# Performance work log

Measured on AMD Instinct MI355X. Metric: run time of the kernel, lower is better.

Reference implementation:

```python
import jax, jax.numpy as jnp
import numpy as np
from jax import lax

V, E, H = 10000, 512, 512
B, L, T = 128, 8, 48


def setup_inputs() -> dict:
    key = jax.random.key(0)
    ks = jax.random.split(key, 12)
    s = lambda k, shape: jax.random.normal(k, shape, jnp.float32) * 0.05
    kw_lens = jnp.sort(jax.random.randint(ks[2], (B,), 1, L + 1))[::-1]  # descending, as pack_padded requires
    return {
        "kws": jax.random.randint(ks[0], (B, L), 0, V),
        "poem": jax.random.randint(ks[1], (B, T), 0, V),
        "kw_lens": kw_lens,
        "embedding": s(ks[3], (V, E)),
        "enc_Wih": s(ks[4], (4 * H, E)), "enc_Whh": s(ks[5], (4 * H, H)), "enc_b": s(ks[6], (4 * H,)),
        "dec_Wih": s(ks[7], (4 * H, E)), "dec_Whh": s(ks[8], (4 * H, H)), "dec_b": s(ks[9], (4 * H,)),
        "out_W": s(ks[10], (V, 2 * H)), "out_b": s(ks[11], (V,)),
    }


def _lstm_step(h, c, x, Wih, Whh, b):
    # PyTorch gate order: i, f, g, o
    gates = x @ Wih.T + h @ Whh.T + b  # [B, 4H]
    i, f, g, o = jnp.split(gates, 4, axis=-1)
    c = jax.nn.sigmoid(f) * c + jax.nn.sigmoid(i) * jnp.tanh(g)
    h = jax.nn.sigmoid(o) * jnp.tanh(c)
    return h, c


def reference(kws, poem, kw_lens, embedding, enc_Wih, enc_Whh, enc_b,
              dec_Wih, dec_Whh, dec_b, out_W, out_b):
    bs = kws.shape[0]
    mask = jnp.arange(L)[None, :] < kw_lens[:, None]  # sequence_mask, [B, L]

    # ---- encoder LSTM over keywords (dropout inactive at eval) ----
    kws_emb = embedding[kws]  # [B, L, E]

    def enc_scan(carry, x):
        h, c = carry
        h, c = _lstm_step(h, c, x, enc_Wih, enc_Whh, enc_b)
        return (h, c), (h, c)

    z = jnp.zeros((bs, H), embedding.dtype)
    _, (hs, cs) = lax.scan(enc_scan, (z, z), kws_emb.transpose(1, 0, 2))  # [L, B, H]
    kws_rep = hs.transpose(1, 0, 2) * mask[..., None]  # pad_packed zeros past length
    # pack semantics: final hidden is the state at the last valid timestep
    bidx = jnp.arange(bs)
    h0 = hs[kw_lens - 1, bidx]
    c0 = cs[kw_lens - 1, bidx]

    # ---- greedy per-timestep decode with dot-product attention ----
    neg = jnp.asarray(-1e9, embedding.dtype)

    def dec_scan(carry, tok):
        h, c = carry
        x = embedding[tok]  # [B, E]
        h, c = _lstm_step(h, c, x, dec_Wih, dec_Whh, dec_b)
        scores = jnp.einsum('bh,blh->bl', h, kws_rep)
        attn = jax.nn.softmax(jnp.where(mask, scores, neg), axis=-1)
        ctx = jnp.einsum('bl,blh->bh', attn, kws_rep)
        logits = jnp.concatenate([h, ctx], axis=-1) @ out_W.T + out_b  # [B, V]
        return (h, c), logits

    _, preds = lax.scan(dec_scan, (h0, c0), poem.T)  # [T, B, V]
    return preds.transpose(1, 0, 2)  # [B, T, V]
```

## Files before the change

kernel.cpp:

```cpp
#include <hip/hip_runtime.h>
#include <hip/hip_bf16.h>

typedef __bf16 bf16;
typedef __attribute__((ext_vector_type(8))) __bf16 bf16x8;
typedef __attribute__((ext_vector_type(4))) __bf16 bf16x4;
typedef __attribute__((ext_vector_type(4))) float f32x4;

#define B_ 128
#define L_ 8
#define T_ 48
#define V_ 10000
#define NBLK_REC 32

__device__ __forceinline__ float sigf(float x) { return 1.f / (1.f + expf(-x)); }

__device__ __forceinline__ void gl_lds16(const bf16* g, bf16* l) {
  __builtin_amdgcn_global_load_lds(
      (const __attribute__((address_space(1))) unsigned int*)g,
      (__attribute__((address_space(3))) unsigned int*)l, 16, 0, 0);
}

__device__ __forceinline__ unsigned aload32(const void* p) {
  return __hip_atomic_load((unsigned*)p, __ATOMIC_RELAXED, __HIP_MEMORY_SCOPE_AGENT);
}
__device__ __forceinline__ void astore64(void* p, unsigned long long v) {
  __hip_atomic_store((unsigned long long*)p, v, __ATOMIC_RELAXED, __HIP_MEMORY_SCOPE_AGENT);
}
__device__ __forceinline__ float bflo(unsigned u) { return __uint_as_float(u << 16); }
__device__ __forceinline__ float bfhi(unsigned u) { return __uint_as_float(u & 0xffff0000u); }
__device__ __forceinline__ unsigned packbf(float lo, float hi) {
  bf16 a = (bf16)lo, b = (bf16)hi;
  unsigned short ua = __builtin_bit_cast(unsigned short, a);
  unsigned short ub = __builtin_bit_cast(unsigned short, b);
  return (unsigned)ua | ((unsigned)ub << 16);
}

__device__ __forceinline__ void signal(unsigned* flg, int blk, unsigned step) {
  asm volatile("s_waitcnt vmcnt(0)" ::: "memory");
  __syncthreads();
  if (threadIdx.x == 0)
    __hip_atomic_store(flg + blk * 32, step, __ATOMIC_RELAXED, __HIP_MEMORY_SCOPE_AGENT);
}
__device__ __forceinline__ void waitstep(const unsigned* flg, unsigned step) {
  if (threadIdx.x < 64) {
    int lane = threadIdx.x;
    for (;;) {
      unsigned v = (lane < NBLK_REC) ? aload32(flg + lane * 32) : step;
      if (__all((int)(v >= step))) break;
      __builtin_amdgcn_s_sleep(1);
    }
  }
  __syncthreads();
}

__global__ void prep_kernel(
    const int* __restrict__ kws, const int* __restrict__ poem,
    const float* __restrict__ emb,
    const float* __restrict__ eWih, const float* __restrict__ eWhh,
    const float* __restrict__ dWih, const float* __restrict__ dWhh,
    const float* __restrict__ outW,
    bf16* __restrict__ WihE, bf16* __restrict__ WhhE,
    bf16* __restrict__ WihD, bf16* __restrict__ WhhD,
    bf16* __restrict__ outWb,
    bf16* __restrict__ Xenc, bf16* __restrict__ Xdec,
    unsigned* __restrict__ flg)
{
  if (blockIdx.x == 0)
    for (int i = threadIdx.x; i < 1024; i += blockDim.x) flg[i] = 0u;
  const long SW = 1048576;
  const long SOWP = 10354688;
  const long SXE = 524288;
  const long SXD = 3145728;
  const long total = 4 * SW + SOWP + SXE + SXD;
  for (long i = blockIdx.x * (long)blockDim.x + threadIdx.x; i < total;
       i += (long)gridDim.x * blockDim.x) {
    long j = i;
    if (j < SW) { WihE[j] = (bf16)eWih[j]; continue; } j -= SW;
    if (j < SW) { WhhE[j] = (bf16)eWhh[j]; continue; } j -= SW;
    if (j < SW) { WihD[j] = (bf16)dWih[j]; continue; } j -= SW;
    if (j < SW) { WhhD[j] = (bf16)dWhh[j]; continue; } j -= SW;
    if (j < SOWP) {
      long r = j >> 10;
      outWb[j] = (r < 10000) ? (bf16)outW[j] : (bf16)0.f;
      continue;
    } j -= SOWP;
    if (j < SXE) {
      int e = (int)(j & 511); int b = (int)((j >> 9) & 127); int l = (int)(j >> 16);
      int tok = kws[b * L_ + l];
      Xenc[j] = (bf16)emb[(long)tok * 512 + e];
      continue;
    } j -= SXE;
    {
      int e = (int)(j & 511); int b = (int)((j >> 9) & 127); int t = (int)(j >> 16);
      int tok = poem[b * T_ + t];
      Xdec[j] = (bf16)emb[(long)tok * 512 + e];
    }
  }
}

template<int MODE>
__global__ __launch_bounds__(256) void gemm2_kernel(
    const bf16* __restrict__ A, const bf16* __restrict__ Bm,
    const float* __restrict__ bias, void* __restrict__ outp,
    int M, int N, int K, int MT)
{
  __shared__ bf16 As[128 * 32];
  __shared__ bf16 Bs[128 * 32];
  const int tid = threadIdx.x, lane = tid & 63, wid = tid >> 6;
  const int nwg = gridDim.x;
  int bid = blockIdx.x;
  int tm, tn;
  if (MODE == 2) {
    int xcd = bid & 7, idx = bid >> 3;
    tm = xcd * 6 + idx % 6;
    tn = idx / 6;
  } else {
    int swz = ((nwg & 7) == 0) ? ((bid & 7) * (nwg >> 3) + (bid >> 3)) : bid;
    tm = swz % MT; tn = swz / MT;
  }
  const int m0 = tm * 128, n0 = tn * 128;
  const int wm = (wid >> 1) * 64, wn = (wid & 1) * 64;
  const int fr = lane & 15, ku = lane >> 4;

  f32x4 acc[4][4];
  #pragma unroll
  for (int mi = 0; mi < 4; ++mi)
    #pragma unroll
    for (int ni = 0; ni < 4; ++ni) {
      acc[mi][ni][0] = 0.f; acc[mi][ni][1] = 0.f;
      acc[mi][ni][2] = 0.f; acc[mi][ni][3] = 0.f;
    }

  for (int kt = 0; kt < K; kt += 32) {
    #pragma unroll
    for (int j = 0; j < 2; ++j) {
      int i0 = j * 256 + wid * 64;
      int i = i0 + lane;
      int r = i >> 2, ub = i & 3;
      gl_lds16(A + (size_t)(m0 + r) * K + kt + ub * 8, As + (size_t)i0 * 8);
      gl_lds16(Bm + (size_t)(n0 + r) * K + kt + ub * 8, Bs + (size_t)i0 * 8);
    }
    __syncthreads();
    bf16x8 af[4], bfr[4];
    #pragma unroll
    for (int mi = 0; mi < 4; ++mi)
      af[mi] = *(const bf16x8*)(As + (size_t)(wm + mi * 16 + fr) * 32 + ku * 8);
    #pragma unroll
    for (int ni = 0; ni < 4; ++ni)
      bfr[ni] = *(const bf16x8*)(Bs + (size_t)(wn + ni * 16 + fr) * 32 + ku * 8);
    #pragma unroll
    for (int mi = 0; mi < 4; ++mi)
      #pragma unroll
      for (int ni = 0; ni < 4; ++ni)
        acc[mi][ni] = __builtin_amdgcn_mfma_f32_16x16x32_bf16(af[mi], bfr[ni], acc[mi][ni], 0, 0, 0);
    __syncthreads();
  }

  const int fq = (lane >> 4) * 4;
  #pragma unroll
  for (int mi = 0; mi < 4; ++mi) {
    #pragma unroll
    for (int ni = 0; ni < 4; ++ni) {
      #pragma unroll
      for (int j = 0; j < 4; ++j) {
        int r = m0 + wm + mi * 16 + fq + j;
        int cix = n0 + wn + ni * 16 + fr;
        if (cix < N) {
          float v = acc[mi][ni][j] + bias[cix];
          if (MODE == 2) {
            int b = r & 127, t = r >> 7;
            ((float*)outp)[(size_t)b * (T_ * V_) + (size_t)t * V_ + cix] = v;
          } else {
            ((bf16*)outp)[((size_t)(r >> 7) * 2048 + cix) * 128 + (r & 127)] = (bf16)v;
          }
        }
      }
    }
  }
}

__global__ __launch_bounds__(256, 1) void recurrent_kernel(
    const bf16* __restrict__ preEncT, const bf16* __restrict__ preDecT,
    const bf16* __restrict__ WhhE, const bf16* __restrict__ WhhD,
    const int* __restrict__ kwl,
    bf16* __restrict__ hS,
    bf16* __restrict__ h0b,
    bf16* __restrict__ hsEnc,
    bf16* __restrict__ Hcat,
    unsigned* __restrict__ flg)
{
  __shared__ bf16 Bs[64 * 512];
  __shared__ bf16 As[128 * 256];
  const int tid = threadIdx.x, lane = tid & 63, wid = tid >> 6;
  const int blk = blockIdx.x, n0 = blk * 16;
  const int fr = lane & 15, fq = (lane >> 4) * 4, ku = lane >> 4;
  const int axor = fr & 7;
  const int arow0 = wid * 32 + fr, arow1 = wid * 32 + 16 + fr;
  const int row0 = wid * 32 + fq, row1 = wid * 32 + 16 + fq;
  const int brow = tid >> 1, bhalf = tid & 1;
  const int blen = kwl[brow];
  const int batt = blk * 4 + wid;
  const int lenb = kwl[batt];
  int lenr[2][4];
  #pragma unroll
  for (int j = 0; j < 4; ++j) { lenr[0][j] = kwl[row0 + j]; lenr[1][j] = kwl[row1 + j]; }

  auto loadB = [&](const bf16* W) {
    #pragma unroll
    for (int j = 0; j < 16; ++j) {
      int i = j * 256 + tid;
      int r = i >> 6, u = i & 63;
      int p = u ^ (r & 7);
      bf16x8 v = *(const bf16x8*)(W + (size_t)((r >> 4) * 512 + n0 + (r & 15)) * 512 + u * 8);
      *(bf16x8*)(Bs + (size_t)r * 512 + p * 8) = v;
    }
  };

  f32x4 acc[2][4];
  auto zacc = [&]() {
    #pragma unroll
    for (int mi = 0; mi < 2; ++mi)
      #pragma unroll
      for (int g = 0; g < 4; ++g) {
        acc[mi][g][0] = 0.f; acc[mi][g][1] = 0.f;
        acc[mi][g][2] = 0.f; acc[mi][g][3] = 0.f;
      }
  };

  auto gemm_full = [&](const bf16* h_in) {
    #pragma unroll
    for (int ch = 0; ch < 2; ++ch) {
      f32x4 tv[16];
      #pragma unroll
      for (int j = 0; j < 16; ++j) {
        int i = j * 256 + tid;
        int r = i >> 5, up = i & 31;
        const bf16* ga = h_in + (size_t)r * 512 + ch * 256 + up * 8;
        asm volatile("global_load_dwordx4 %0, %1, off sc0 sc1"
                     : "=v"(tv[j]) : "v"(ga) : "memory");
      }
      asm volatile("s_waitcnt vmcnt(0)" ::: "memory");
      __builtin_amdgcn_sched_barrier(0);
      #pragma unroll
      for (int j = 0; j < 16; ++j) {
        int i = j * 256 + tid;
        int r = i >> 5, up = i & 31;
        int s = up ^ (r & 7);
        *(f32x4*)(As + ((size_t)r * 32 + s) * 8) = tv[j];
      }
      __syncthreads();
      #pragma unroll
      for (int kt = 0; kt < 8; ++kt) {
        int cA = (kt * 4 + ku) ^ axor;
        int cB = ((ch * 8 + kt) * 4 + ku) ^ axor;
        bf16x8 af0 = *(const bf16x8*)(As + (size_t)arow0 * 256 + cA * 8);
        bf16x8 af1 = *(const bf16x8*)(As + (size_t)arow1 * 256 + cA * 8);
        #pragma unroll
        for (int g = 0; g < 4; ++g) {
          bf16x8 bv = *(const bf16x8*)(Bs + (size_t)(g * 16 + fr) * 512 + cB * 8);
          acc[0][g] = __builtin_amdgcn_mfma_f32_16x16x32_bf16(af0, bv, acc[0][g], 0, 0, 0);
          acc[1][g] = __builtin_amdgcn_mfma_f32_16x16x32_bf16(af1, bv, acc[1][g], 0, 0, 0);
        }
      }
      __syncthreads();
    }
  };

  float cr[2][4] = {{0.f,0.f,0.f,0.f},{0.f,0.f,0.f,0.f}};
  float c0r[2][4] = {{0.f,0.f,0.f,0.f},{0.f,0.f,0.f,0.f}};
  bf16 hout[2][4];

  bf16x4 gv[2][4];
  auto prefg = [&](const bf16* preT) {
    #pragma unroll
    for (int mi = 0; mi < 2; ++mi) {
      int rbase = mi ? row1 : row0;
      int hcol = n0 + fr;
      #pragma unroll
      for (int g = 0; g < 4; ++g)
        gv[mi][g] = *(const bf16x4*)(preT + ((size_t)(g * 512 + hcol)) * 128 + rbase);
    }
  };

  auto pointwise = [&]() {
    #pragma unroll
    for (int mi = 0; mi < 2; ++mi) {
      #pragma unroll
      for (int j = 0; j < 4; ++j) {
        float gi = acc[mi][0][j] + (float)gv[mi][0][j];
        float gf = acc[mi][1][j] + (float)gv[mi][1][j];
        float gg = acc[mi][2][j] + (float)gv[mi][2][j];
        float go = acc[mi][3][j] + (float)gv[mi][3][j];
        float cn = sigf(gf) * cr[mi][j] + sigf(gi) * tanhf(gg);
        float hn = sigf(go) * tanhf(cn);
        cr[mi][j] = cn;
        hout[mi][j] = (bf16)hn;
      }
    }
  };

  auto bounce_store = [&](bf16* hdst, bf16* hsdst, int t, int is_enc) {
    #pragma unroll
    for (int mi = 0; mi < 2; ++mi) {
      int rbase = mi ? row1 : row0;
      #pragma unroll
      for (int j = 0; j < 4; ++j)
        As[(size_t)(rbase + j) * 16 + fr] = hout[mi][j];
    }
    __syncthreads();
    unsigned long long v0 = *(unsigned long long*)(As + (size_t)brow * 16 + bhalf * 8);
    unsigned long long v1 = *(unsigned long long*)(As + (size_t)brow * 16 + bhalf * 8 + 4);
    size_t off = (size_t)brow * 512 + n0 + bhalf * 8;
    astore64(hdst + off, v0);
    astore64(hdst + off + 4, v1);
    if (is_enc) {
      unsigned long long m0 = (t < blen) ? v0 : 0ull;
      unsigned long long m1 = (t < blen) ? v1 : 0ull;
      astore64(hsdst + off, m0);
      astore64(hsdst + off + 4, m1);
      if (t == blen - 1) {
        astore64(h0b + off, v0);
        astore64(h0b + off + 4, v1);
      }
    }
  };

  unsigned hatt[4];
  auto load_hatt = [&](const bf16* h_in) {
    #pragma unroll
    for (int e = 0; e < 4; ++e)
      hatt[e] = aload32(h_in + (size_t)batt * 512 + lane * 2 + 128 * e);
  };

  unsigned hsr[8][4];

  auto attention = [&](int tprev) {
    float sc[8];
    #pragma unroll
    for (int l = 0; l < 8; ++l) {
      float p = 0.f;
      #pragma unroll
      for (int e = 0; e < 4; ++e)
        p += bflo(hatt[e]) * bflo(hsr[l][e]) + bfhi(hatt[e]) * bfhi(hsr[l][e]);
      #pragma unroll
      for (int off = 32; off; off >>= 1) p += __shfl_xor(p, off);
      sc[l] = p;
    }
    float m = -1e30f;
    #pragma unroll
    for (int l = 0; l < 8; ++l) m = fmaxf(m, (l < lenb) ? sc[l] : -1e30f);
    float wgt[8]; float den = 0.f;
    #pragma unroll
    for (int l = 0; l < 8; ++l) { wgt[l] = (l < lenb) ? expf(sc[l] - m) : 0.f; den += wgt[l]; }
    float inv = 1.f / den;
    bf16* dst = Hcat + ((size_t)tprev * 128 + batt) * 1024;
    #pragma unroll
    for (int e = 0; e < 4; ++e) {
      float clo = 0.f, chi = 0.f;
      #pragma unroll
      for (int l = 0; l < 8; ++l) {
        clo += wgt[l] * bflo(hsr[l][e]);
        chi += wgt[l] * bfhi(hsr[l][e]);
      }
      *(unsigned*)(dst + 512 + lane * 2 + 128 * e) = packbf(clo * inv, chi * inv);
      *(unsigned*)(dst + lane * 2 + 128 * e) = hatt[e];
    }
  };

  loadB(WhhE);
  __syncthreads();
  for (int t = 0; t < 8; ++t) {
    prefg(preEncT + (size_t)t * 262144);
    zacc();
    if (t > 0) {
      waitstep(flg, (unsigned)t);
      gemm_full(hS + (size_t)(t - 1) * 65536);
    }
    pointwise();
    #pragma unroll
    for (int mi = 0; mi < 2; ++mi)
      #pragma unroll
      for (int j = 0; j < 4; ++j)
        if (t == lenr[mi][j] - 1) c0r[mi][j] = cr[mi][j];
    bounce_store(hS + (size_t)t * 65536, hsEnc + (size_t)t * 65536, t, 1);
    signal(flg, blk, (unsigned)(t + 1));
  }

  __syncthreads();
  loadB(WhhD);
  __syncthreads();
  waitstep(flg, 8u);
  #pragma unroll
  for (int l = 0; l < 8; ++l)
    #pragma unroll
    for (int e = 0; e < 4; ++e)
      hsr[l][e] = aload32(hsEnc + ((size_t)l * 128 + batt) * 512 + lane * 2 + 128 * e);
  #pragma unroll
  for (int mi = 0; mi < 2; ++mi)
    #pragma unroll
    for (int j = 0; j < 4; ++j) cr[mi][j] = c0r[mi][j];

  for (int t = 0; t < 48; ++t) {
    prefg(preDecT + (size_t)t * 262144);
    zacc();
    const bf16* hin = (t == 0) ? (const bf16*)h0b : (const bf16*)(hS + (size_t)(8 + t - 1) * 65536);
    waitstep(flg, (unsigned)(8 + t));
    gemm_full(hin);
    pointwise();
    bounce_store(hS + (size_t)(8 + t) * 65536, nullptr, t, 0);
    signal(flg, blk, (unsigned)(9 + t));
    if (t >= 1) {
      load_hatt(hin);
      attention(t - 1);
    }
  }
  waitstep(flg, 56u);
  load_hatt(hS + (size_t)55 * 65536);
  attention(47);
}

extern "C" void kernel_launch(void* const* d_in, const int* in_sizes, int n_in,
                              void* d_out, int out_size, void* d_ws, size_t ws_size,
                              hipStream_t stream)
{
  const int* kws  = (const int*)d_in[0];
  const int* poem = (const int*)d_in[1];
  const int* kwl  = (const int*)d_in[2];
  const float* emb  = (const float*)d_in[3];
  const float* eWih = (const float*)d_in[4];
  const float* eWhh = (const float*)d_in[5];
  const float* eb   = (const float*)d_in[6];
  const float* dWih = (const float*)d_in[7];
  const float* dWhh = (const float*)d_in[8];
  const float* db   = (const float*)d_in[9];
  const float* outW = (const float*)d_in[10];
  const float* outb = (const float*)d_in[11];
  float* out = (float*)d_out;

  char* base = (char*)d_ws;
  size_t o = 0;
  auto take = [&](size_t bytes) -> char* {
    char* r = base + o;
    o += (bytes + 255) & ~(size_t)255;
    return r;
  };
  bf16* WihE  = (bf16*)take(2048 * 512 * 2);
  bf16* WhhE  = (bf16*)take(2048 * 512 * 2);
  bf16* WihD  = (bf16*)take(2048 * 512 * 2);
  bf16* WhhD  = (bf16*)take(2048 * 512 * 2);
  bf16* outWb = (bf16*)take((size_t)10112 * 1024 * 2);
  bf16* Xenc  = (bf16*)take(1024 * 512 * 2);
  bf16* Xdec  = (bf16*)take((size_t)6144 * 512 * 2);
  bf16* preEncT = (bf16*)take((size_t)8 * 2048 * 128 * 2);
  bf16* preDecT = (bf16*)take((size_t)48 * 2048 * 128 * 2);
  bf16* Hcat   = (bf16*)take((size_t)6144 * 1024 * 2);
  bf16* hS     = (bf16*)take((size_t)56 * 65536 * 2);
  bf16* hsEnc  = (bf16*)take((size_t)8 * 128 * 512 * 2);
  bf16* h0b    = (bf16*)take(128 * 512 * 2);
  unsigned* flg = (unsigned*)take(4096);

  prep_kernel<<<4096, 256, 0, stream>>>(kws, poem, emb, eWih, eWhh, dWih, dWhh, outW,
                                        WihE, WhhE, WihD, WhhD, outWb, Xenc, Xdec, flg);

  gemm2_kernel<3><<<128, 256, 0, stream>>>(Xenc, WihE, eb, preEncT, 1024, 2048, 512, 8);
  gemm2_kernel<3><<<768, 256, 0, stream>>>(Xdec, WihD, db, preDecT, 6144, 2048, 512, 48);

  recurrent_kernel<<<NBLK_REC, 256, 0, stream>>>(preEncT, preDecT, WhhE, WhhD, kwl,
                                                 hS, h0b, hsEnc, Hcat, flg);

  gemm2_kernel<2><<<3792, 256, 0, stream>>>(Hcat, outWb, outb, out, 6144, 10000, 1024, 48);
}
```

Measured before the change: 788.1 us.

## Fuse decoder input GEMM and output projection into persistent recurrent kernel

Merges the decoder input-projection GEMM and the vocabulary output GEMM into the recurrent kernel. The kernel launches 240 blocks: 32 run the LSTM recurrence and 208 worker blocks first compute preDecT and then stream the output-logit tiles per timestep as soon as that step's Hcat rows are flagged complete. The goal is to overlap the large output GEMM and the decoder pre-GEMM with the latency-bound serial recurrence, and to remove kernel launch gaps. In exchange it relies on all 240 blocks being co-resident for the spin-wait flags, and the worker GEMM loses the XCD-aware tile swizzle and uses a simpler unpipelined load path.

```diff
diff --git a/kernel.cpp b/kernel.cpp
--- a/kernel.cpp
+++ b/kernel.cpp
@@ -11,6 +11,8 @@
 #define T_ 48
 #define V_ 10000
 #define NBLK_REC 32
+#define NBLK_TOT 240
+#define NW (NBLK_TOT - NBLK_REC)
 
 __device__ __forceinline__ float sigf(float x) { return 1.f / (1.f + expf(-x)); }
 
@@ -33,24 +35,6 @@
   unsigned short ua = __builtin_bit_cast(unsigned short, a);
   unsigned short ub = __builtin_bit_cast(unsigned short, b);
   return (unsigned)ua | ((unsigned)ub << 16);
-}
-
-__device__ __forceinline__ void signal(unsigned* flg, int blk, unsigned step) {
-  asm volatile("s_waitcnt vmcnt(0)" ::: "memory");
-  __syncthreads();
-  if (threadIdx.x == 0)
-    __hip_atomic_store(flg + blk * 32, step, __ATOMIC_RELAXED, __HIP_MEMORY_SCOPE_AGENT);
-}
-__device__ __forceinline__ void waitstep(const unsigned* flg, unsigned step) {
-  if (threadIdx.x < 64) {
-    int lane = threadIdx.x;
-    for (;;) {
-      unsigned v = (lane < NBLK_REC) ? aload32(flg + lane * 32) : step;
-      if (__all((int)(v >= step))) break;
-      __builtin_amdgcn_s_sleep(1);
-    }
-  }
-  __syncthreads();
 }
 
 __global__ void prep_kernel(
@@ -63,10 +47,10 @@
     bf16* __restrict__ WihD, bf16* __restrict__ WhhD,
     bf16* __restrict__ outWb,
     bf16* __restrict__ Xenc, bf16* __restrict__ Xdec,
-    unsigned* __restrict__ flg)
+    unsigned* __restrict__ ctl)
 {
   if (blockIdx.x == 0)
-    for (int i = threadIdx.x; i < 1024; i += blockDim.x) flg[i] = 0u;
+    for (int i = threadIdx.x; i < 8192; i += blockDim.x) ctl[i] = 0u;
   const long SW = 1048576;
   const long SOWP = 10354688;
   const long SXE = 524288;
@@ -98,10 +82,9 @@
   }
 }
 
-template<int MODE>
-__global__ __launch_bounds__(256) void gemm2_kernel(
+__global__ __launch_bounds__(256) void gemm_pre_kernel(
     const bf16* __restrict__ A, const bf16* __restrict__ Bm,
-    const float* __restrict__ bias, void* __restrict__ outp,
+    const float* __restrict__ bias, bf16* __restrict__ outp,
     int M, int N, int K, int MT)
 {
   __shared__ bf16 As[128 * 32];
@@ -109,15 +92,8 @@
   const int tid = threadIdx.x, lane = tid & 63, wid = tid >> 6;
   const int nwg = gridDim.x;
   int bid = blockIdx.x;
-  int tm, tn;
-  if (MODE == 2) {
-    int xcd = bid & 7, idx = bid >> 3;
-    tm = xcd * 6 + idx % 6;
-    tn = idx / 6;
-  } else {
-    int swz = ((nwg & 7) == 0) ? ((bid & 7) * (nwg >> 3) + (bid >> 3)) : bid;
-    tm = swz % MT; tn = swz / MT;
-  }
+  int swz = ((nwg & 7) == 0) ? ((bid & 7) * (nwg >> 3) + (bid >> 3)) : bid;
+  const int tm = swz % MT, tn = swz / MT;
   const int m0 = tm * 128, n0 = tn * 128;
   const int wm = (wid >> 1) * 64, wn = (wid & 1) * 64;
   const int fr = lane & 15, ku = lane >> 4;
@@ -165,258 +141,454 @@
       for (int j = 0; j < 4; ++j) {
         int r = m0 + wm + mi * 16 + fq + j;
         int cix = n0 + wn + ni * 16 + fr;
-        if (cix < N) {
-          float v = acc[mi][ni][j] + bias[cix];
-          if (MODE == 2) {
-            int b = r & 127, t = r >> 7;
-            ((float*)outp)[(size_t)b * (T_ * V_) + (size_t)t * V_ + cix] = v;
-          } else {
-            ((bf16*)outp)[((size_t)(r >> 7) * 2048 + cix) * 128 + (r & 127)] = (bf16)v;
-          }
-        }
+        outp[((size_t)(r >> 7) * 2048 + cix) * 128 + (r & 127)] = (bf16)(acc[mi][ni][j] + bias[cix]);
       }
     }
   }
 }
 
-__global__ __launch_bounds__(256, 1) void recurrent_kernel(
-    const bf16* __restrict__ preEncT, const bf16* __restrict__ preDecT,
+__global__ __launch_bounds__(256, 1) void fused_kernel(
+    const bf16* __restrict__ preEncT, bf16* __restrict__ preDecT,
     const bf16* __restrict__ WhhE, const bf16* __restrict__ WhhD,
     const int* __restrict__ kwl,
-    bf16* __restrict__ hS,
-    bf16* __restrict__ h0b,
-    bf16* __restrict__ hsEnc,
-    bf16* __restrict__ Hcat,
-    unsigned* __restrict__ flg)
+    bf16* __restrict__ hS, bf16* __restrict__ h0b,
+    bf16* __restrict__ hsEnc, bf16* __restrict__ Hcat,
+    const bf16* __restrict__ Xdec, const bf16* __restrict__ WihD,
+    const float* __restrict__ db, const bf16* __restrict__ outWb,
+    const float* __restrict__ outb, float* __restrict__ out,
+    unsigned* __restrict__ ctl)
 {
-  __shared__ bf16 Bs[64 * 512];
-  __shared__ bf16 As[128 * 256];
+  __shared__ __align__(16) char pool[131072];
   const int tid = threadIdx.x, lane = tid & 63, wid = tid >> 6;
-  const int blk = blockIdx.x, n0 = blk * 16;
-  const int fr = lane & 15, fq = (lane >> 4) * 4, ku = lane >> 4;
-  const int axor = fr & 7;
-  const int arow0 = wid * 32 + fr, arow1 = wid * 32 + 16 + fr;
-  const int row0 = wid * 32 + fq, row1 = wid * 32 + 16 + fq;
-  const int brow = tid >> 1, bhalf = tid & 1;
-  const int blen = kwl[brow];
-  const int batt = blk * 4 + wid;
-  const int lenb = kwl[batt];
-  int lenr[2][4];
-  #pragma unroll
-  for (int j = 0; j < 4; ++j) { lenr[0][j] = kwl[row0 + j]; lenr[1][j] = kwl[row1 + j]; }
-
-  auto loadB = [&](const bf16* W) {
-    #pragma unroll
-    for (int j = 0; j < 16; ++j) {
-      int i = j * 256 + tid;
-      int r = i >> 6, u = i & 63;
-      int p = u ^ (r & 7);
-      bf16x8 v = *(const bf16x8*)(W + (size_t)((r >> 4) * 512 + n0 + (r & 15)) * 512 + u * 8);
-      *(bf16x8*)(Bs + (size_t)r * 512 + p * 8) = v;
-    }
-  };
-
-  f32x4 acc[2][4];
-  auto zacc = [&]() {
-    #pragma unroll
-    for (int mi = 0; mi < 2; ++mi)
-      #pragma unroll
-      for (int g = 0; g < 4; ++g) {
-        acc[mi][g][0] = 0.f; acc[mi][g][1] = 0.f;
-        acc[mi][g][2] = 0.f; acc[mi][g][3] = 0.f;
-      }
-  };
-
-  auto gemm_full = [&](const bf16* h_in) {
-    #pragma unroll
-    for (int ch = 0; ch < 2; ++ch) {
-      f32x4 tv[16];
+
+  if (blockIdx.x < NBLK_REC) {
+    bf16* Bs = (bf16*)pool;
+    bf16* As = (bf16*)(pool + 65536);
+    unsigned* flg = ctl;
+    const int blk = blockIdx.x, n0 = blk * 16;
+    const int fr = lane & 15, fq = (lane >> 4) * 4, ku = lane >> 4;
+    const int axor = fr & 7;
+    const int arow0 = wid * 32 + fr, arow1 = wid * 32 + 16 + fr;
+    const int row0 = wid * 32 + fq, row1 = wid * 32 + 16 + fq;
+    const int brow = tid >> 1, bhalf = tid & 1;
+    const int blen = kwl[brow];
+    const int batt = blk * 4 + wid;
+    const int lenb = kwl[batt];
+    int lenr[2][4];
+    #pragma unroll
+    for (int j = 0; j < 4; ++j) { lenr[0][j] = kwl[row0 + j]; lenr[1][j] = kwl[row1 + j]; }
+
+    auto signal = [&](unsigned step) {
+      asm volatile("s_waitcnt vmcnt(0)" ::: "memory");
+      __syncthreads();
+      if (tid == 0)
+        __hip_atomic_store(flg + blk * 32, step, __ATOMIC_RELAXED, __HIP_MEMORY_SCOPE_AGENT);
+    };
+    auto waitstep = [&](unsigned step) {
+      if (tid < 64) {
+        int l = tid;
+        for (;;) {
+          unsigned v = (l < NBLK_REC) ? aload32(flg + l * 32) : step;
+          if (__all((int)(v >= step))) break;
+          __builtin_amdgcn_s_sleep(1);
+        }
+      }
+      __syncthreads();
+    };
+
+    auto loadB = [&](const bf16* W) {
       #pragma unroll
       for (int j = 0; j < 16; ++j) {
         int i = j * 256 + tid;
-        int r = i >> 5, up = i & 31;
-        const bf16* ga = h_in + (size_t)r * 512 + ch * 256 + up * 8;
-        asm volatile("global_load_dwordx4 %0, %1, off sc0 sc1"
-                     : "=v"(tv[j]) : "v"(ga) : "memory");
-      }
+        int r = i >> 6, u = i & 63;
+        int p = u ^ (r & 7);
+        bf16x8 v = *(const bf16x8*)(W + (size_t)((r >> 4) * 512 + n0 + (r & 15)) * 512 + u * 8);
+        *(bf16x8*)(Bs + (size_t)r * 512 + p * 8) = v;
+      }
+    };
+
+    f32x4 acc[2][4];
+    auto zacc = [&]() {
+      #pragma unroll
+      for (int mi = 0; mi < 2; ++mi)
+        #pragma unroll
+        for (int g = 0; g < 4; ++g) {
+          acc[mi][g][0] = 0.f; acc[mi][g][1] = 0.f;
+          acc[mi][g][2] = 0.f; acc[mi][g][3] = 0.f;
+        }
+    };
+
+    auto gemm_full = [&](const bf16* h_in) {
+      #pragma unroll
+      for (int ch = 0; ch < 2; ++ch) {
+        f32x4 tv[16];
+        #pragma unroll
+        for (int j = 0; j < 16; ++j) {
+          int i = j * 256 + tid;
+          int r = i >> 5, up = i & 31;
+          const bf16* ga = h_in + (size_t)r * 512 + ch * 256 + up * 8;
+          asm volatile("global_load_dwordx4 %0, %1, off sc0 sc1"
+                       : "=v"(tv[j]) : "v"(ga) : "memory");
+        }
+        asm volatile("s_waitcnt vmcnt(0)" ::: "memory");
+        __builtin_amdgcn_sched_barrier(0);
+        #pragma unroll
+        for (int j = 0; j < 16; ++j) {
+          int i = j * 256 + tid;
+          int r = i >> 5, up = i & 31;
+          int s = up ^ (r & 7);
+          *(f32x4*)(As + ((size_t)r * 32 + s) * 8) = tv[j];
+        }
+        __syncthreads();
+        #pragma unroll
+        for (int kt = 0; kt < 8; ++kt) {
+          int cA = (kt * 4 + ku) ^ axor;
+          int cB = ((ch * 8 + kt) * 4 + ku) ^ axor;
+          bf16x8 af0 = *(const bf16x8*)(As + (size_t)arow0 * 256 + cA * 8);
+          bf16x8 af1 = *(const bf16x8*)(As + (size_t)arow1 * 256 + cA * 8);
+          #pragma unroll
+          for (int g = 0; g < 4; ++g) {
+            bf16x8 bv = *(const bf16x8*)(Bs + (size_t)(g * 16 + fr) * 512 + cB * 8);
+            acc[0][g] = __builtin_amdgcn_mfma_f32_16x16x32_bf16(af0, bv, acc[0][g], 0, 0, 0);
+            acc[1][g] = __builtin_amdgcn_mfma_f32_16x16x32_bf16(af1, bv, acc[1][g], 0, 0, 0);
+          }
+        }
+        __syncthreads();
+      }
+    };
+
+    float cr[2][4] = {{0.f,0.f,0.f,0.f},{0.f,0.f,0.f,0.f}};
+    float c0r[2][4] = {{0.f,0.f,0.f,0.f},{0.f,0.f,0.f,0.f}};
+    bf16 hout[2][4];
+    bf16x4 gv[2][4];
+
+    auto prefg = [&](const bf16* preT) {
+      #pragma unroll
+      for (int mi = 0; mi < 2; ++mi) {
+        int rbase = mi ? row1 : row0;
+        int hcol = n0 + fr;
+        #pragma unroll
+        for (int g = 0; g < 4; ++g)
+          gv[mi][g] = *(const bf16x4*)(preT + ((size_t)(g * 512 + hcol)) * 128 + rbase);
+      }
+    };
+    auto prefg_c = [&](const bf16* preT) {
+      #pragma unroll
+      for (int mi = 0; mi < 2; ++mi) {
+        int rbase = mi ? row1 : row0;
+        int hcol = n0 + fr;
+        #pragma unroll
+        for (int g = 0; g < 4; ++g) {
+          const bf16* p = preT + ((size_t)(g * 512 + hcol)) * 128 + rbase;
+          unsigned long long u;
+          asm volatile("global_load_dwordx2 %0, %1, off sc0 sc1" : "=v"(u) : "v"(p) : "memory");
+          gv[mi][g] = __builtin_bit_cast(bf16x4, u);
+        }
+      }
+    };
+
+    auto pointwise = [&]() {
+      #pragma unroll
+      for (int mi = 0; mi < 2; ++mi) {
+        #pragma unroll
+        for (int j = 0; j < 4; ++j) {
+          float gi = acc[mi][0][j] + (float)gv[mi][0][j];
+          float gf = acc[mi][1][j] + (float)gv[mi][1][j];
+          float gg = acc[mi][2][j] + (float)gv[mi][2][j];
+          float go = acc[mi][3][j] + (float)gv[mi][3][j];
+          float cn = sigf(gf) * cr[mi][j] + sigf(gi) * tanhf(gg);
+          float hn = sigf(go) * tanhf(cn);
+          cr[mi][j] = cn;
+          hout[mi][j] = (bf16)hn;
+        }
+      }
+    };
+
+    auto bounce_store = [&](bf16* hdst, bf16* hsdst, int t, int is_enc) {
+      #pragma unroll
+      for (int mi = 0; mi < 2; ++mi) {
+        int rbase = mi ? row1 : row0;
+        #pragma unroll
+        for (int j = 0; j < 4; ++j)
+          As[(size_t)(rbase + j) * 16 + fr] = hout[mi][j];
+      }
+      __syncthreads();
+      unsigned long long v0 = *(unsigned long long*)(As + (size_t)brow * 16 + bhalf * 8);
+      unsigned long long v1 = *(unsigned long long*)(As + (size_t)brow * 16 + bhalf * 8 + 4);
+      size_t off = (size_t)brow * 512 + n0 + bhalf * 8;
+      astore64(hdst + off, v0);
+      astore64(hdst + off + 4, v1);
+      if (is_enc) {
+        unsigned long long m0 = (t < blen) ? v0 : 0ull;
+        unsigned long long m1 = (t < blen) ? v1 : 0ull;
+        astore64(hsdst + off, m0);
+        astore64(hsdst + off + 4, m1);
+        if (t == blen - 1) {
+          astore64(h0b + off, v0);
+          astore64(h0b + off + 4, v1);
+        }
+      }
+    };
+
+    unsigned hatt[4];
+    auto load_hatt = [&](const bf16* h_in) {
+      #pragma unroll
+      for (int e = 0; e < 4; ++e) {
+        const bf16* p = h_in + (size_t)batt * 512 + lane * 2 + 128 * e;
+        asm volatile("global_load_dword %0, %1, off sc0 sc1" : "=v"(hatt[e]) : "v"(p) : "memory");
+      }
+    };
+
+    unsigned hsr[8][4];
+
+    auto attention = [&](int tprev) {
       asm volatile("s_waitcnt vmcnt(0)" ::: "memory");
       __builtin_amdgcn_sched_barrier(0);
-      #pragma unroll
-      for (int j = 0; j < 16; ++j) {
-        int i = j * 256 + tid;
-        int r = i >> 5, up = i & 31;
-        int s = up ^ (r & 7);
-        *(f32x4*)(As + ((size_t)r * 32 + s) * 8) = tv[j];
-      }
-      __syncthreads();
-      #pragma unroll
-      for (int kt = 0; kt < 8; ++kt) {
-        int cA = (kt * 4 + ku) ^ axor;
-        int cB = ((ch * 8 + kt) * 4 + ku) ^ axor;
-        bf16x8 af0 = *(const bf16x8*)(As + (size_t)arow0 * 256 + cA * 8);
-        bf16x8 af1 = *(const bf16x8*)(As + (size_t)arow1 * 256 + cA * 8);
-        #pragma unroll
-        for (int g = 0; g < 4; ++g) {
-          bf16x8 bv = *(const bf16x8*)(Bs + (size_t)(g * 16 + fr) * 512 + cB * 8);
-          acc[0][g] = __builtin_amdgcn_mfma_f32_16x16x32_bf16(af0, bv, acc[0][g], 0, 0, 0);
-          acc[1][g] = __builtin_amdgcn_mfma_f32_16x16x32_bf16(af1, bv, acc[1][g], 0, 0, 0);
-        }
-      }
-      __syncthreads();
-    }
-  };
-
-  float cr[2][4] = {{0.f,0.f,0.f,0.f},{0.f,0.f,0.f,0.f}};
-  float c0r[2][4] = {{0.f,0.f,0.f,0.f},{0.f,0.f,0.f,0.f}};
-  bf16 hout[2][4];
-
-  bf16x4 gv[2][4];
-  auto prefg = [&](const bf16* preT) {
-    #pragma unroll
-    for (int mi = 0; mi < 2; ++mi) {
-      int rbase = mi ? row1 : row0;
-      int hcol = n0 + fr;
-      #pragma unroll
-      for (int g = 0; g < 4; ++g)
-        gv[mi][g] = *(const bf16x4*)(preT + ((size_t)(g * 512 + hcol)) * 128 + rbase);
-    }
-  };
-
-  auto pointwise = [&]() {
-    #pragma unroll
-    for (int mi = 0; mi < 2; ++mi) {
-      #pragma unroll
-      for (int j = 0; j < 4; ++j) {
-        float gi = acc[mi][0][j] + (float)gv[mi][0][j];
-        float gf = acc[mi][1][j] + (float)gv[mi][1][j];
-        float gg = acc[mi][2][j] + (float)gv[mi][2][j];
-        float go = acc[mi][3][j] + (float)gv[mi][3][j];
-        float cn = sigf(gf) * cr[mi][j] + sigf(gi) * tanhf(gg);
-        float hn = sigf(go) * tanhf(cn);
-        cr[mi][j] = cn;
-        hout[mi][j] = (bf16)hn;
-      }
-    }
-  };
-
-  auto bounce_store = [&](bf16* hdst, bf16* hsdst, int t, int is_enc) {
-    #pragma unroll
-    for (int mi = 0; mi < 2; ++mi) {
-      int rbase = mi ? row1 : row0;
-      #pragma unroll
-      for (int j = 0; j < 4; ++j)
-        As[(size_t)(rbase + j) * 16 + fr] = hout[mi][j];
-    }
+      float sc[8];
+      #pragma unroll
+      for (int l = 0; l < 8; ++l) {
+        float p = 0.f;
+        #pragma unroll
+        for (int e = 0; e < 4; ++e)
+          p += bflo(hatt[e]) * bflo(hsr[l][e]) + bfhi(hatt[e]) * bfhi(hsr[l][e]);
+        #pragma unroll
+        for (int off = 32; off; off >>= 1) p += __shfl_xor(p, off);
+        sc[l] = p;
+      }
+      float m = -1e30f;
+      #pragma unroll
+      for (int l = 0; l < 8; ++l) m = fmaxf(m, (l < lenb) ? sc[l] : -1e30f);
+      float wgt[8]; float den = 0.f;
+      #pragma unroll
+      for (int l = 0; l < 8; ++l) { wgt[l] = (l < lenb) ? expf(sc[l] - m) : 0.f; den += wgt[l]; }
+      float inv = 1.f / den;
+      bf16* dst = Hcat + ((size_t)tprev * 128 + batt) * 1024;
+      #pragma unroll
+      for (int e = 0; e < 4; ++e) {
+        float clo = 0.f, chi = 0.f;
+        #pragma unroll
+        for (int l = 0; l < 8; ++l) {
+          clo += wgt[l] * bflo(hsr[l][e]);
+          chi += wgt[l] * bfhi(hsr[l][e]);
+        }
+        unsigned cw = packbf(clo * inv, chi * inv);
+        unsigned* d1 = (unsigned*)(dst + 512 + lane * 2 + 128 * e);
+        unsigned* d0 = (unsigned*)(dst + lane * 2 + 128 * e);
+        asm volatile("global_store_dword %0, %1, off sc0 sc1" :: "v"(d1), "v"(cw) : "memory");
+        asm volatile("global_store_dword %0, %1, off sc0 sc1" :: "v"(d0), "v"(hatt[e]) : "memory");
+      }
+    };
+
+    auto hcat_done = [&](int t) {
+      asm volatile("s_waitcnt vmcnt(0)" ::: "memory");
+      __syncthreads();
+      if (tid == 0)
+        __hip_atomic_fetch_add(ctl + 1056 + t * 32, 1u, __ATOMIC_RELAXED, __HIP_MEMORY_SCOPE_AGENT);
+    };
+
+    loadB(WhhE);
     __syncthreads();
-    unsigned long long v0 = *(unsigned long long*)(As + (size_t)brow * 16 + bhalf * 8);
-    unsigned long long v1 = *(unsigned long long*)(As + (size_t)brow * 16 + bhalf * 8 + 4);
-    size_t off = (size_t)brow * 512 + n0 + bhalf * 8;
-    astore64(hdst + off, v0);
-    astore64(hdst + off + 4, v1);
-    if (is_enc) {
-      unsigned long long m0 = (t < blen) ? v0 : 0ull;
-      unsigned long long m1 = (t < blen) ? v1 : 0ull;
-      astore64(hsdst + off, m0);
-      astore64(hsdst + off + 4, m1);
-      if (t == blen - 1) {
-        astore64(h0b + off, v0);
-        astore64(h0b + off + 4, v1);
-      }
-    }
-  };
-
-  unsigned hatt[4];
-  auto load_hatt = [&](const bf16* h_in) {
-    #pragma unroll
-    for (int e = 0; e < 4; ++e)
-      hatt[e] = aload32(h_in + (size_t)batt * 512 + lane * 2 + 128 * e);
-  };
-
-  unsigned hsr[8][4];
-
-  auto attention = [&](int tprev) {
-    float sc[8];
-    #pragma unroll
-    for (int l = 0; l < 8; ++l) {
-      float p = 0.f;
+    for (int t = 0; t < 8; ++t) {
+      prefg(preEncT + (size_t)t * 262144);
+      zacc();
+      if (t > 0) {
+        waitstep((unsigned)t);
+        gemm_full(hS + (size_t)(t - 1) * 65536);
+      }
+      pointwise();
+      #pragma unroll
+      for (int mi = 0; mi < 2; ++mi)
+        #pragma unroll
+        for (int j = 0; j < 4; ++j)
+          if (t == lenr[mi][j] - 1) c0r[mi][j] = cr[mi][j];
+      bounce_store(hS + (size_t)t * 65536, hsEnc + (size_t)t * 65536, t, 1);
+      signal((unsigned)(t + 1));
+    }
+
+    __syncthreads();
+    loadB(WhhD);
+    __syncthreads();
+    waitstep(8u);
+    #pragma unroll
+    for (int l = 0; l < 8; ++l)
       #pragma unroll
       for (int e = 0; e < 4; ++e)
-        p += bflo(hatt[e]) * bflo(hsr[l][e]) + bfhi(hatt[e]) * bfhi(hsr[l][e]);
-      #pragma unroll
-      for (int off = 32; off; off >>= 1) p += __shfl_xor(p, off);
-      sc[l] = p;
-    }
-    float m = -1e30f;
-    #pragma unroll
-    for (int l = 0; l < 8; ++l) m = fmaxf(m, (l < lenb) ? sc[l] : -1e30f);
-    float wgt[8]; float den = 0.f;
-    #pragma unroll
-    for (int l = 0; l < 8; ++l) { wgt[l] = (l < lenb) ? expf(sc[l] - m) : 0.f; den += wgt[l]; }
-    float inv = 1.f / den;
-    bf16* dst = Hcat + ((size_t)tprev * 128 + batt) * 1024;
-    #pragma unroll
-    for (int e = 0; e < 4; ++e) {
-      float clo = 0.f, chi = 0.f;
-      #pragma unroll
-      for (int l = 0; l < 8; ++l) {
-        clo += wgt[l] * bflo(hsr[l][e]);
-        chi += wgt[l] * bfhi(hsr[l][e]);
-      }
-      *(unsigned*)(dst + 512 + lane * 2 + 128 * e) = packbf(clo * inv, chi * inv);
-      *(unsigned*)(dst + lane * 2 + 128 * e) = hatt[e];
-    }
-  };
-
-  loadB(WhhE);
-  __syncthreads();
-  for (int t = 0; t < 8; ++t) {
-    prefg(preEncT + (size_t)t * 262144);
-    zacc();
-    if (t > 0) {
-      waitstep(flg, (unsigned)t);
-      gemm_full(hS + (size_t)(t - 1) * 65536);
-    }
-    pointwise();
+        hsr[l][e] = aload32(hsEnc + ((size_t)l * 128 + batt) * 512 + lane * 2 + 128 * e);
     #pragma unroll
     for (int mi = 0; mi < 2; ++mi)
       #pragma unroll
-      for (int j = 0; j < 4; ++j)
-        if (t == lenr[mi][j] - 1) c0r[mi][j] = cr[mi][j];
-    bounce_store(hS + (size_t)t * 65536, hsEnc + (size_t)t * 65536, t, 1);
-    signal(flg, blk, (unsigned)(t + 1));
+      for (int j = 0; j < 4; ++j) cr[mi][j] = c0r[mi][j];
+    if (tid == 0) {
+      unsigned v; int it = 0;
+      do {
+        asm volatile("global_load_dword %0, %1, off sc0 sc1\ns_waitcnt vmcnt(0)"
+                     : "=v"(v) : "v"(ctl + 1024) : "memory");
+        if (v >= 768u) break;
+        __builtin_amdgcn_s_sleep(4);
+      } while (++it < (1 << 20));
+    }
+    __syncthreads();
+
+    for (int t = 0; t < 48; ++t) {
+      prefg_c(preDecT + (size_t)t * 262144);
+      zacc();
+      const bf16* hin = (t == 0) ? (const bf16*)h0b
+                                 : (const bf16*)(hS + (size_t)(8 + t - 1) * 65536);
+      waitstep((unsigned)(8 + t));
+      gemm_full(hin);
+      pointwise();
+      bounce_store(hS + (size_t)(8 + t) * 65536, nullptr, t, 0);
+      signal((unsigned)(9 + t));
+      if (t >= 1) {
+        load_hatt(hin);
+        attention(t - 1);
+        hcat_done(t - 1);
+      }
+    }
+    waitstep(56u);
+    load_hatt(hS + (size_t)55 * 65536);
+    attention(47);
+    hcat_done(47);
+
+  } else {
+    bf16* AsW = (bf16*)pool;
+    bf16* BsW = (bf16*)(pool + 8192);
+    bf16* Tb  = (bf16*)(pool + 16384);
+    const int w = blockIdx.x - NBLK_REC;
+    const int fr = lane & 15, ku = lane >> 4;
+    const int wm = (wid >> 1) * 64, wn = (wid & 1) * 64;
+    const int fq = (lane >> 4) * 4;
+
+    f32x4 acc[4][4];
+    auto zacc = [&]() {
+      #pragma unroll
+      for (int mi = 0; mi < 4; ++mi)
+        #pragma unroll
+        for (int ni = 0; ni < 4; ++ni) {
+          acc[mi][ni][0] = 0.f; acc[mi][ni][1] = 0.f;
+          acc[mi][ni][2] = 0.f; acc[mi][ni][3] = 0.f;
+        }
+    };
+    auto mfma_iter = [&]() {
+      bf16x8 af[4], bfr[4];
+      #pragma unroll
+      for (int mi = 0; mi < 4; ++mi)
+        af[mi] = *(const bf16x8*)(AsW + (size_t)(wm + mi * 16 + fr) * 32 + ku * 8);
+      #pragma unroll
+      for (int ni = 0; ni < 4; ++ni)
+        bfr[ni] = *(const bf16x8*)(BsW + (size_t)(wn + ni * 16 + fr) * 32 + ku * 8);
+      #pragma unroll
+      for (int mi = 0; mi < 4; ++mi)
+        #pragma unroll
+        for (int ni = 0; ni < 4; ++ni)
+          acc[mi][ni] = __builtin_amdgcn_mfma_f32_16x16x32_bf16(af[mi], bfr[ni], acc[mi][ni], 0, 0, 0);
+    };
+    auto wait_ge = [&](unsigned* p, unsigned target) {
+      if (tid == 0) {
+        unsigned v; int it = 0;
+        do {
+          asm volatile("global_load_dword %0, %1, off sc0 sc1\ns_waitcnt vmcnt(0)"
+                       : "=v"(v) : "v"(p) : "memory");
+          if (v >= target) break;
+          __builtin_amdgcn_s_sleep(8);
+        } while (++it < (1 << 20));
+      }
+      __syncthreads();
+    };
+
+    for (int i = w; i < 768; i += NW) {
+      int t = i >> 4, tn = i & 15;
+      int m0 = t * 128, n0 = tn * 128;
+      zacc();
+      for (int kt = 0; kt < 512; kt += 32) {
+        #pragma unroll
+        for (int j = 0; j < 2; ++j) {
+          int i0 = j * 256 + wid * 64;
+          int ii = i0 + lane;
+          int r = ii >> 2, q = ii & 3;
+          gl_lds16(Xdec + (size_t)(m0 + r) * 512 + kt + q * 8, AsW + (size_t)i0 * 8);
+          gl_lds16(WihD + (size_t)(n0 + r) * 512 + kt + q * 8, BsW + (size_t)i0 * 8);
+        }
+        __syncthreads();
+        mfma_iter();
+        __syncthreads();
+      }
+      #pragma unroll
+      for (int mi = 0; mi < 4; ++mi)
+        #pragma unroll
+        for (int ni = 0; ni < 4; ++ni) {
+          int cl = wn + ni * 16 + fr;
+          float bias = db[n0 + cl];
+          #pragma unroll
+          for (int j = 0; j < 4; ++j)
+            Tb[(size_t)cl * 128 + (wm + mi * 16 + fq + j)] = (bf16)(acc[mi][ni][j] + bias);
+        }
+      __syncthreads();
+      #pragma unroll
+      for (int rep = 0; rep < 8; ++rep) {
+        int u = rep * 256 + tid;
+        int cl = u >> 4, cb = u & 15;
+        f32x4 v = *(f32x4*)(Tb + (size_t)cl * 128 + cb * 8);
+        bf16* dst = preDecT + ((size_t)t * 2048 + n0 + cl) * 128 + cb * 8;
+        asm volatile("global_store_dwordx4 %0, %1, off sc0 sc1" :: "v"(dst), "v"(v) : "memory");
+      }
+      asm volatile("s_waitcnt vmcnt(0)" ::: "memory");
+      __syncthreads();
+      if (tid == 0)
+        __hip_atomic_fetch_add(ctl + 1024, 1u, __ATOMIC_RELAXED, __HIP_MEMORY_SCOPE_AGENT);
+      __syncthreads();
+    }
+
+    int seen = -1;
+    for (int i = w; i < 3792; i += NW) {
+      int t = i / 79, n = i % 79;
+      if (t > seen) { wait_ge(ctl + 1056 + t * 32, (unsigned)NBLK_REC); seen = t; }
+      int n0 = n * 128;
+      zacc();
+      for (int kt = 0; kt < 1024; kt += 32) {
+        f32x4 v0, v1;
+        {
+          int u = tid, r = u >> 2, q = u & 3;
+          const bf16* pa = Hcat + ((size_t)t * 128 + r) * 1024 + kt + q * 8;
+          asm volatile("global_load_dwordx4 %0, %1, off sc0 sc1" : "=v"(v0) : "v"(pa) : "memory");
+        }
+        {
+          int u = tid + 256, r = u >> 2, q = u & 3;
+          const bf16* pa = Hcat + ((size_t)t * 128 + r) * 1024 + kt + q * 8;
+          asm volatile("global_load_dwordx4 %0, %1, off sc0 sc1" : "=v"(v1) : "v"(pa) : "memory");
+        }
+        #pragma unroll
+        for (int j = 0; j < 2; ++j) {
+          int i0 = j * 256 + wid * 64;
+          int ii = i0 + lane;
+          int r = ii >> 2, q = ii & 3;
+          gl_lds16(outWb + (size_t)(n0 + r) * 1024 + kt + q * 8, BsW + (size_t)i0 * 8);
+        }
+        asm volatile("s_waitcnt vmcnt(0)" ::: "memory");
+        __builtin_amdgcn_sched_barrier(0);
+        *(f32x4*)(AsW + (size_t)tid * 8) = v0;
+        *(f32x4*)(AsW + ((size_t)tid + 256) * 8) = v1;
+        __syncthreads();
+        mfma_iter();
+        __syncthreads();
+      }
+      #pragma unroll
+      for (int mi = 0; mi < 4; ++mi) {
+        #pragma unroll
+        for (int ni = 0; ni < 4; ++ni) {
+          int cix = n0 + wn + ni * 16 + fr;
+          if (cix < V_) {
+            float bias = outb[cix];
+            #pragma unroll
+            for (int j = 0; j < 4; ++j) {
+              int b = wm + mi * 16 + fq + j;
+              out[(size_t)b * (T_ * V_) + (size_t)t * V_ + cix] = acc[mi][ni][j] + bias;
+            }
+          }
+        }
+      }
+    }
   }
-
-  __syncthreads();
-  loadB(WhhD);
-  __syncthreads();
-  waitstep(flg, 8u);
-  #pragma unroll
-  for (int l = 0; l < 8; ++l)
-    #pragma unroll
-    for (int e = 0; e < 4; ++e)
-      hsr[l][e] = aload32(hsEnc + ((size_t)l * 128 + batt) * 512 + lane * 2 + 128 * e);
-  #pragma unroll
-  for (int mi = 0; mi < 2; ++mi)
-    #pragma unroll
-    for (int j = 0; j < 4; ++j) cr[mi][j] = c0r[mi][j];
-
-  for (int t = 0; t < 48; ++t) {
-    prefg(preDecT + (size_t)t * 262144);
-    zacc();
-    const bf16* hin = (t == 0) ? (const bf16*)h0b : (const bf16*)(hS + (size_t)(8 + t - 1) * 65536);
-    waitstep(flg, (unsigned)(8 + t));
-    gemm_full(hin);
-    pointwise();
-    bounce_store(hS + (size_t)(8 + t) * 65536, nullptr, t, 0);
-    signal(flg, blk, (unsigned)(9 + t));
-    if (t >= 1) {
-      load_hatt(hin);
-      attention(t - 1);
-    }
-  }
-  waitstep(flg, 56u);
-  load_hatt(hS + (size_t)55 * 65536);
-  attention(47);
 }
 
 extern "C" void kernel_launch(void* const* d_in, const int* in_sizes, int n_in,
@@ -457,16 +629,14 @@
   bf16* hS     = (bf16*)take((size_t)56 * 65536 * 2);
   bf16* hsEnc  = (bf16*)take((size_t)8 * 128 * 512 * 2);
   bf16* h0b    = (bf16*)take(128 * 512 * 2);
-  unsigned* flg = (unsigned*)take(4096);
+  unsigned* ctl = (unsigned*)take(32768);
 
   prep_kernel<<<4096, 256, 0, stream>>>(kws, poem, emb, eWih, eWhh, dWih, dWhh, outW,
-                                        WihE, WhhE, WihD, WhhD, outWb, Xenc, Xdec, flg);
-
-  gemm2_kernel<3><<<128, 256, 0, stream>>>(Xenc, WihE, eb, preEncT, 1024, 2048, 512, 8);
-  gemm2_kernel<3><<<768, 256, 0, stream>>>(Xdec, WihD, db, preDecT, 6144, 2048, 512, 48);
-
-  recurrent_kernel<<<NBLK_REC, 256, 0, stream>>>(preEncT, preDecT, WhhE, WhhD, kwl,
-                                                 hS, h0b, hsEnc, Hcat, flg);
-
-  gemm2_kernel<2><<<3792, 256, 0, stream>>>(Hcat, outWb, outb, out, 6144, 10000, 1024, 48);
-}
+                                        WihE, WhhE, WihD, WhhD, outWb, Xenc, Xdec, ctl);
+
+  gemm_pre_kernel<<<128, 256, 0, stream>>>(Xenc, WihE, eb, preEncT, 1024, 2048, 512, 8);
+
+  fused_kernel<<<NBLK_TOT, 256, 0, stream>>>(preEncT, preDecT, WhhE, WhhD, kwl,
+                                             hS, h0b, hsEnc, Hcat,
+                                             Xdec, WihD, db, outWb, outb, out, ctl);
+}
```

New measurement: 720.4 us. -8.6%, faster.
